# Performance work log

Measured on AMD Instinct MI355X. Metric: run time of the kernel, lower is better.

The kernel has to match this reference:

```python
import jax, jax.numpy as jnp
import numpy as np

N_NODES = 100000
N_EDGES = 1000000
N_BATCH = 64
D = 64            # node/edge/global feature dim
IN_DIM = 3 * D    # node + agg_received_edges + global
LATENT = 32
OUT_DIM = 64


def setup_inputs() -> dict:
    key = jax.random.key(0)
    ks = jax.random.split(key, 9)
    return {
        "node_attr": jax.random.normal(ks[0], (N_NODES, D), dtype=jnp.float32),
        "edge_attr": jax.random.normal(ks[1], (N_EDGES, D), dtype=jnp.float32),
        "global_attr": jax.random.normal(ks[2], (N_BATCH, D), dtype=jnp.float32),
        "W1": jax.random.normal(ks[3], (IN_DIM, LATENT), dtype=jnp.float32) * (1.0 / np.sqrt(IN_DIM)),
        "b1": jnp.zeros((LATENT,), dtype=jnp.float32),
        "W2": jax.random.normal(ks[4], (LATENT, OUT_DIM), dtype=jnp.float32) * (1.0 / np.sqrt(LATENT)),
        "b2": jnp.zeros((OUT_DIM,), dtype=jnp.float32),
        "receivers_idx": jax.random.randint(ks[5], (N_EDGES,), 0, N_NODES, dtype=jnp.int32),
        "ng_index": jax.random.randint(ks[6], (N_NODES,), 0, N_BATCH, dtype=jnp.int32),
    }


def scatter_mean(src, index, num_segments):
    # segment-sum then divide by count (count clamped to 1 where empty -> mean=0)
    sums = jax.ops.segment_sum(src, index, num_segments=num_segments)
    cnt = jax.ops.segment_sum(jnp.ones((src.shape[0],), src.dtype), index,
                              num_segments=num_segments)
    return sums / jnp.maximum(cnt, 1.0)[:, None]


def reference(node_attr, edge_attr, global_attr, W1, b1, W2, b2,
              receivers_idx, ng_index):
    num_nodes = node_attr.shape[0]
    # aggregated received-edge features per node  [N, D]
    agg_received = scatter_mean(edge_attr, receivers_idx, num_nodes)
    # gather per-node global attrs               [N, D]
    expanded_global = global_attr[ng_index]
    # concat -> small MLP                        [N, 3D] -> [N, out_dim]
    collected = jnp.concatenate([node_attr, agg_received, expanded_global], axis=-1)
    h = jax.nn.relu(collected @ W1 + b1)
    return h @ W2 + b2
```

## Files before the change

### kernel.cpp

```cpp
#include <hip/hip_runtime.h>

#define DD 64
#define LATENT 32
#define OUTD 64
#define CAP 64

typedef float vfloat4 __attribute__((ext_vector_type(4)));

__global__ __launch_bounds__(256) void bin_kernel(
    const int* __restrict__ recv, int* __restrict__ counts,
    int* __restrict__ slots, int nEdges)
{
    int e = blockIdx.x * 256 + threadIdx.x;
    if (e < nEdges) {
        int r = recv[e];
        int rank = atomicAdd(&counts[r], 1);
        if (rank < CAP) slots[((size_t)r << 6) + rank] = e;
    }
}

__global__ __launch_bounds__(256) void g1_kernel(
    const float* __restrict__ global_attr,
    const float* __restrict__ W1,
    const float* __restrict__ b1,
    float*       __restrict__ g1,
    int nBatch)
{
    int t = blockIdx.x * 256 + threadIdx.x;
    int b = t >> 5;
    int j = t & 31;
    if (b >= nBatch) return;
    float acc = b1[j];
    const float* g = global_attr + (size_t)b * DD;
    const float* w = W1 + 128 * LATENT + j;
    for (int k = 0; k < DD; ++k)
        acc = fmaf(g[k], w[k * LATENT], acc);
    g1[b * LATENT + j] = acc;
}

__global__ __launch_bounds__(256) void gather_kernel(
    const float* __restrict__ edge_attr,
    const int*   __restrict__ slots,
    const int*   __restrict__ counts,
    float*       __restrict__ mean_out,
    int nNodes)
{
    int node = (blockIdx.x * 256 + threadIdx.x) >> 6;
    int lane = threadIdx.x & 63;
    if (node >= nNodes) return;
    const int g = lane >> 4;
    const int s = lane & 15;

    const int cnt = counts[node];
    const int lim = min(cnt, CAP);
    const int* row = slots + ((size_t)node << 6);

    int myid = row[min(lane, max(lim - 1, 0))];

    vfloat4 acc = {0.f, 0.f, 0.f, 0.f};
    for (int i = 0; i < lim; i += 16) {
        int ia = min(i + g,      lim - 1);
        int ib = min(i + 4 + g,  lim - 1);
        int ic = min(i + 8 + g,  lim - 1);
        int id_ = min(i + 12 + g, lim - 1);
        int eA = __shfl(myid, ia, 64);
        int eB = __shfl(myid, ib, 64);
        int eC = __shfl(myid, ic, 64);
        int eD = __shfl(myid, id_, 64);
        vfloat4 a = {0.f,0.f,0.f,0.f}, b = a, c = a, d = a;
        if (i + g < lim)
            a = __builtin_nontemporal_load(((const vfloat4*)(edge_attr + (size_t)eA * DD)) + s);
        if (i + 4 + g < lim)
            b = __builtin_nontemporal_load(((const vfloat4*)(edge_attr + (size_t)eB * DD)) + s);
        if (i + 8 + g < lim)
            c = __builtin_nontemporal_load(((const vfloat4*)(edge_attr + (size_t)eC * DD)) + s);
        if (i + 12 + g < lim)
            d = __builtin_nontemporal_load(((const vfloat4*)(edge_attr + (size_t)eD * DD)) + s);
        acc += a; acc += b; acc += c; acc += d;
    }

    acc.x += __shfl_xor(acc.x, 16, 64);
    acc.y += __shfl_xor(acc.y, 16, 64);
    acc.z += __shfl_xor(acc.z, 16, 64);
    acc.w += __shfl_xor(acc.w, 16, 64);
    acc.x += __shfl_xor(acc.x, 32, 64);
    acc.y += __shfl_xor(acc.y, 32, 64);
    acc.z += __shfl_xor(acc.z, 32, 64);
    acc.w += __shfl_xor(acc.w, 32, 64);

    if (g == 0) {
        float inv = 1.0f / (float)max(cnt, 1);
        vfloat4 r = {acc.x * inv, acc.y * inv, acc.z * inv, acc.w * inv};
        ((vfloat4*)(mean_out + (size_t)node * DD))[s] = r;
    }
}

__global__ __launch_bounds__(128) void mlp_kernel(
    const float* __restrict__ node_attr,
    const int*   __restrict__ ng_index,
    const float* __restrict__ W1,
    const float* __restrict__ W2,
    const float* __restrict__ b2,
    const float* __restrict__ g1,
    float*                    io,
    int nNodes)
{
    __shared__ float slab[2][64 * 65];

    const int wave = threadIdx.x >> 6;
    const int lane = threadIdx.x & 63;
    const int base = blockIdx.x * 128 + wave * 64;
    if (base >= nNodes) return;
    const int nvalid = min(64, nNodes - base);
    float* S = slab[wave];

    float h[LATENT];
    {
        const int n = base + (lane < nvalid ? lane : 0);
        const int g = ng_index[n];
        const float4* gp = (const float4*)(g1 + g * LATENT);
#pragma unroll
        for (int q = 0; q < 8; ++q) {
            float4 gv = gp[q];
            h[4*q+0] = gv.x; h[4*q+1] = gv.y;
            h[4*q+2] = gv.z; h[4*q+3] = gv.w;
        }
    }

#pragma unroll 8
    for (int r = 0; r < nvalid; ++r)
        S[r * 65 + lane] = node_attr[(size_t)(base + r) * DD + lane];
    {
        const float* w = W1;
#pragma unroll 8
        for (int k = 0; k < DD; ++k) {
            float x = S[lane * 65 + k];
            const float* wr = w + k * LATENT;
#pragma unroll
            for (int j = 0; j < LATENT; ++j)
                h[j] = fmaf(x, wr[j], h[j]);
        }
    }

#pragma unroll 8
    for (int r = 0; r < nvalid; ++r)
        S[r * 65 + lane] = io[(size_t)(base + r) * DD + lane];
    {
        const float* w = W1 + DD * LATENT;
#pragma unroll 8
        for (int k = 0; k < DD; ++k) {
            float x = S[lane * 65 + k];
            const float* wr = w + k * LATENT;
#pragma unroll
            for (int j = 0; j < LATENT; ++j)
                h[j] = fmaf(x, wr[j], h[j]);
        }
    }

#pragma unroll
    for (int j = 0; j < LATENT; ++j) h[j] = fmaxf(h[j], 0.0f);

#pragma unroll
    for (int c = 0; c < 2; ++c) {
        float o[32];
#pragma unroll
        for (int t = 0; t < 32; ++t) o[t] = b2[c * 32 + t];
        for (int j = 0; j < LATENT; ++j) {
            const float hj = h[j];
            const float* wr = W2 + j * OUTD + c * 32;
#pragma unroll
            for (int t = 0; t < 32; ++t) o[t] = fmaf(hj, wr[t], o[t]);
        }
#pragma unroll
        for (int t = 0; t < 32; ++t) S[lane * 65 + c * 32 + t] = o[t];
    }

#pragma unroll 8
    for (int r = 0; r < nvalid; ++r)
        io[(size_t)(base + r) * DD + lane] = S[r * 65 + lane];
}

extern "C" void kernel_launch(void* const* d_in, const int* in_sizes, int n_in,
                              void* d_out, int out_size, void* d_ws, size_t ws_size,
                              hipStream_t stream)
{
    const float* node_attr   = (const float*)d_in[0];
    const float* edge_attr   = (const float*)d_in[1];
    const float* global_attr = (const float*)d_in[2];
    const float* W1          = (const float*)d_in[3];
    const float* b1          = (const float*)d_in[4];
    const float* W2          = (const float*)d_in[5];
    const float* b2          = (const float*)d_in[6];
    const int*   recv        = (const int*)d_in[7];
    const int*   ng_index    = (const int*)d_in[8];
    float*       out         = (float*)d_out;

    const int nNodes = in_sizes[0] / DD;
    const int nEdges = in_sizes[1] / DD;
    const int nBatch = in_sizes[2] / DD;

    int*   counts = (int*)d_ws;
    int*   slots  = counts + nNodes;
    float* g1     = (float*)(slots + (size_t)nNodes * CAP);

    hipMemsetAsync(counts, 0, (size_t)nNodes * sizeof(int), stream);

    bin_kernel<<<(nEdges + 255) / 256, 256, 0, stream>>>(recv, counts, slots, nEdges);

    g1_kernel<<<(nBatch * LATENT + 255) / 256, 256, 0, stream>>>(
        global_attr, W1, b1, g1, nBatch);

    gather_kernel<<<(nNodes + 3) / 4, 256, 0, stream>>>(
        edge_attr, slots, counts, out, nNodes);

    mlp_kernel<<<(nNodes + 127) / 128, 128, 0, stream>>>(
        node_attr, ng_index, W1, W2, b2, g1, out, nNodes);
}
```

Baseline: 499.7 us.

## Fuse edge gather-mean into MLP kernel and vectorize edge binning

Folds the per-node mean over received edges into the MLP kernel. Each wave now loops over its 64 nodes, accumulates the edge features into shared memory and feeds them straight into the first layer, prefetching the next node's count and slot row as it goes. This drops the round trip of the intermediate mean tensor through global memory and one kernel launch. The binning kernel also handles four edges per thread through an int4 load of receiver indices. The cost is that gather parallelism drops to about 1.5k waves that each walk nodes one after another, which may leave too few loads in flight to hide memory latency.

```diff
diff --git a/kernel.cpp b/kernel.cpp
--- a/kernel.cpp
+++ b/kernel.cpp
@@ -11,11 +11,21 @@
     const int* __restrict__ recv, int* __restrict__ counts,
     int* __restrict__ slots, int nEdges)
 {
-    int e = blockIdx.x * 256 + threadIdx.x;
-    if (e < nEdges) {
-        int r = recv[e];
-        int rank = atomicAdd(&counts[r], 1);
-        if (rank < CAP) slots[((size_t)r << 6) + rank] = e;
+    int t = blockIdx.x * 256 + threadIdx.x;
+    int e0 = t * 4;
+    if (e0 + 3 < nEdges) {
+        int4 r4 = *(const int4*)(recv + e0);
+        int rank;
+        rank = atomicAdd(&counts[r4.x], 1); if (rank < CAP) slots[((size_t)r4.x << 6) + rank] = e0;
+        rank = atomicAdd(&counts[r4.y], 1); if (rank < CAP) slots[((size_t)r4.y << 6) + rank] = e0 + 1;
+        rank = atomicAdd(&counts[r4.z], 1); if (rank < CAP) slots[((size_t)r4.z << 6) + rank] = e0 + 2;
+        rank = atomicAdd(&counts[r4.w], 1); if (rank < CAP) slots[((size_t)r4.w << 6) + rank] = e0 + 3;
+    } else {
+        for (int e = e0; e < nEdges; ++e) {
+            int r = recv[e];
+            int rank = atomicAdd(&counts[r], 1);
+            if (rank < CAP) slots[((size_t)r << 6) + rank] = e;
+        }
     }
 }
 
@@ -38,71 +48,17 @@
     g1[b * LATENT + j] = acc;
 }
 
-__global__ __launch_bounds__(256) void gather_kernel(
+__global__ __launch_bounds__(128) void fused_kernel(
     const float* __restrict__ edge_attr,
     const int*   __restrict__ slots,
     const int*   __restrict__ counts,
-    float*       __restrict__ mean_out,
-    int nNodes)
-{
-    int node = (blockIdx.x * 256 + threadIdx.x) >> 6;
-    int lane = threadIdx.x & 63;
-    if (node >= nNodes) return;
-    const int g = lane >> 4;
-    const int s = lane & 15;
-
-    const int cnt = counts[node];
-    const int lim = min(cnt, CAP);
-    const int* row = slots + ((size_t)node << 6);
-
-    int myid = row[min(lane, max(lim - 1, 0))];
-
-    vfloat4 acc = {0.f, 0.f, 0.f, 0.f};
-    for (int i = 0; i < lim; i += 16) {
-        int ia = min(i + g,      lim - 1);
-        int ib = min(i + 4 + g,  lim - 1);
-        int ic = min(i + 8 + g,  lim - 1);
-        int id_ = min(i + 12 + g, lim - 1);
-        int eA = __shfl(myid, ia, 64);
-        int eB = __shfl(myid, ib, 64);
-        int eC = __shfl(myid, ic, 64);
-        int eD = __shfl(myid, id_, 64);
-        vfloat4 a = {0.f,0.f,0.f,0.f}, b = a, c = a, d = a;
-        if (i + g < lim)
-            a = __builtin_nontemporal_load(((const vfloat4*)(edge_attr + (size_t)eA * DD)) + s);
-        if (i + 4 + g < lim)
-            b = __builtin_nontemporal_load(((const vfloat4*)(edge_attr + (size_t)eB * DD)) + s);
-        if (i + 8 + g < lim)
-            c = __builtin_nontemporal_load(((const vfloat4*)(edge_attr + (size_t)eC * DD)) + s);
-        if (i + 12 + g < lim)
-            d = __builtin_nontemporal_load(((const vfloat4*)(edge_attr + (size_t)eD * DD)) + s);
-        acc += a; acc += b; acc += c; acc += d;
-    }
-
-    acc.x += __shfl_xor(acc.x, 16, 64);
-    acc.y += __shfl_xor(acc.y, 16, 64);
-    acc.z += __shfl_xor(acc.z, 16, 64);
-    acc.w += __shfl_xor(acc.w, 16, 64);
-    acc.x += __shfl_xor(acc.x, 32, 64);
-    acc.y += __shfl_xor(acc.y, 32, 64);
-    acc.z += __shfl_xor(acc.z, 32, 64);
-    acc.w += __shfl_xor(acc.w, 32, 64);
-
-    if (g == 0) {
-        float inv = 1.0f / (float)max(cnt, 1);
-        vfloat4 r = {acc.x * inv, acc.y * inv, acc.z * inv, acc.w * inv};
-        ((vfloat4*)(mean_out + (size_t)node * DD))[s] = r;
-    }
-}
-
-__global__ __launch_bounds__(128) void mlp_kernel(
     const float* __restrict__ node_attr,
     const int*   __restrict__ ng_index,
     const float* __restrict__ W1,
     const float* __restrict__ W2,
     const float* __restrict__ b2,
     const float* __restrict__ g1,
-    float*                    io,
+    float*       __restrict__ out,
     int nNodes)
 {
     __shared__ float slab[2][64 * 65];
@@ -111,42 +67,91 @@
     const int lane = threadIdx.x & 63;
     const int base = blockIdx.x * 128 + wave * 64;
     if (base >= nNodes) return;
-    const int nvalid = min(64, nNodes - base);
+    const int nv = min(64, nNodes - base);
     float* S = slab[wave];
+    const int g = lane >> 4;
+    const int s = lane & 15;
 
     float h[LATENT];
     {
-        const int n = base + (lane < nvalid ? lane : 0);
-        const int g = ng_index[n];
-        const float4* gp = (const float4*)(g1 + g * LATENT);
+        const int n = base + (lane < nv ? lane : 0);
+        const int gb = ng_index[n];
+        const vfloat4* gp = (const vfloat4*)(g1 + gb * LATENT);
 #pragma unroll
         for (int q = 0; q < 8; ++q) {
-            float4 gv = gp[q];
+            vfloat4 gv = gp[q];
             h[4*q+0] = gv.x; h[4*q+1] = gv.y;
             h[4*q+2] = gv.z; h[4*q+3] = gv.w;
         }
     }
 
-#pragma unroll 8
-    for (int r = 0; r < nvalid; ++r)
+    int cnt_n  = counts[base];
+    int myid_n = slots[((size_t)base << 6) + lane];
+    for (int r = 0; r < nv; ++r) {
+        const int cnt  = cnt_n;
+        const int myid = myid_n;
+        if (r + 1 < nv) {
+            cnt_n  = counts[base + r + 1];
+            myid_n = slots[((size_t)(base + r + 1) << 6) + lane];
+        }
+        const int lim = min(cnt, CAP);
+
+        vfloat4 acc = {0.f, 0.f, 0.f, 0.f};
+        for (int i = 0; i < lim; i += 16) {
+            int ia  = min(i + g,      lim - 1);
+            int ib  = min(i + 4 + g,  lim - 1);
+            int ic  = min(i + 8 + g,  lim - 1);
+            int id_ = min(i + 12 + g, lim - 1);
+            int eA = __shfl(myid, ia, 64);
+            int eB = __shfl(myid, ib, 64);
+            int eC = __shfl(myid, ic, 64);
+            int eD = __shfl(myid, id_, 64);
+            vfloat4 a = {0.f,0.f,0.f,0.f}, b = a, c = a, d = a;
+            if (i + g < lim)
+                a = __builtin_nontemporal_load(((const vfloat4*)(edge_attr + (size_t)eA * DD)) + s);
+            if (i + 4 + g < lim)
+                b = __builtin_nontemporal_load(((const vfloat4*)(edge_attr + (size_t)eB * DD)) + s);
+            if (i + 8 + g < lim)
+                c = __builtin_nontemporal_load(((const vfloat4*)(edge_attr + (size_t)eC * DD)) + s);
+            if (i + 12 + g < lim)
+                d = __builtin_nontemporal_load(((const vfloat4*)(edge_attr + (size_t)eD * DD)) + s);
+            acc += a; acc += b; acc += c; acc += d;
+        }
+        acc.x += __shfl_xor(acc.x, 16, 64);
+        acc.y += __shfl_xor(acc.y, 16, 64);
+        acc.z += __shfl_xor(acc.z, 16, 64);
+        acc.w += __shfl_xor(acc.w, 16, 64);
+        acc.x += __shfl_xor(acc.x, 32, 64);
+        acc.y += __shfl_xor(acc.y, 32, 64);
+        acc.z += __shfl_xor(acc.z, 32, 64);
+        acc.w += __shfl_xor(acc.w, 32, 64);
+
+        if (g == 0) {
+            float inv = 1.0f / (float)max(cnt, 1);
+            S[r * 65 + 4*s + 0] = acc.x * inv;
+            S[r * 65 + 4*s + 1] = acc.y * inv;
+            S[r * 65 + 4*s + 2] = acc.z * inv;
+            S[r * 65 + 4*s + 3] = acc.w * inv;
+        }
+    }
+
+    {
+        const float* w = W1 + DD * LATENT;
+#pragma unroll 8
+        for (int k = 0; k < DD; ++k) {
+            float x = S[lane * 65 + k];
+            const float* wr = w + k * LATENT;
+#pragma unroll
+            for (int j = 0; j < LATENT; ++j)
+                h[j] = fmaf(x, wr[j], h[j]);
+        }
+    }
+
+#pragma unroll 8
+    for (int r = 0; r < nv; ++r)
         S[r * 65 + lane] = node_attr[(size_t)(base + r) * DD + lane];
     {
         const float* w = W1;
-#pragma unroll 8
-        for (int k = 0; k < DD; ++k) {
-            float x = S[lane * 65 + k];
-            const float* wr = w + k * LATENT;
-#pragma unroll
-            for (int j = 0; j < LATENT; ++j)
-                h[j] = fmaf(x, wr[j], h[j]);
-        }
-    }
-
-#pragma unroll 8
-    for (int r = 0; r < nvalid; ++r)
-        S[r * 65 + lane] = io[(size_t)(base + r) * DD + lane];
-    {
-        const float* w = W1 + DD * LATENT;
 #pragma unroll 8
         for (int k = 0; k < DD; ++k) {
             float x = S[lane * 65 + k];
@@ -176,8 +181,8 @@
     }
 
 #pragma unroll 8
-    for (int r = 0; r < nvalid; ++r)
-        io[(size_t)(base + r) * DD + lane] = S[r * 65 + lane];
+    for (int r = 0; r < nv; ++r)
+        out[(size_t)(base + r) * DD + lane] = S[r * 65 + lane];
 }
 
 extern "C" void kernel_launch(void* const* d_in, const int* in_sizes, int n_in,
@@ -205,14 +210,11 @@
 
     hipMemsetAsync(counts, 0, (size_t)nNodes * sizeof(int), stream);
 
-    bin_kernel<<<(nEdges + 255) / 256, 256, 0, stream>>>(recv, counts, slots, nEdges);
+    bin_kernel<<<(nEdges + 1023) / 1024, 256, 0, stream>>>(recv, counts, slots, nEdges);
 
     g1_kernel<<<(nBatch * LATENT + 255) / 256, 256, 0, stream>>>(
         global_attr, W1, b1, g1, nBatch);
 
-    gather_kernel<<<(nNodes + 3) / 4, 256, 0, stream>>>(
-        edge_attr, slots, counts, out, nNodes);
-
-    mlp_kernel<<<(nNodes + 127) / 128, 128, 0, stream>>>(
-        node_attr, ng_index, W1, W2, b2, g1, out, nNodes);
-}
+    fused_kernel<<<(nNodes + 127) / 128, 128, 0, stream>>>(
+        edge_attr, slots, counts, node_attr, ng_index, W1, W2, b2, g1, out, nNodes);
+}
```

New measurement: 485.0 us. 1.03x faster.
